# Kernel tuning notes

Hardware: AMD Instinct MI355X
Metric: run time of the kernel (lower is better)

Reference implementation:

```python
import jax, jax.numpy as jnp
import numpy as np

# Group structure (matches init_kwargs)
SIZES = np.array([16]*16 + [32]*32 + [64]*16)          # teacher_embedding_sizes_list
CHOICES = np.array([4]*16 + [8]*32 + [16]*16)          # max_choice_per_embedding
IN_DIM = int(SIZES.sum())                               # 2304
OUT_DIM = int(CHOICES.sum())                            # 576
W_TOTAL = int((SIZES * CHOICES).sum())                  # 25600
BATCH = 16384


def setup_inputs() -> dict:
    key = jax.random.key(0)
    k1, k2 = jax.random.split(key)
    x = jax.random.normal(k1, (BATCH, IN_DIM), dtype=jnp.float32)
    # TruncatedNormal(stddev=0.15) approximated with scaled normal
    weight = jax.random.normal(k2, (W_TOTAL, 1), dtype=jnp.float32) * 0.15
    bias = jnp.zeros((OUT_DIM,), dtype=jnp.float32)
    return {"x": x, "weight": weight, "bias": bias}


def reference(x, weight, bias):
    # Block-diagonal grouped GEMM: per-group slice of x times per-group weight
    # block reshaped to [size_i, choice_i], concatenated along features + bias.
    w_flat = weight[:, 0]
    outs = []
    w_idx = 0
    t_idx = 0
    for size, choice in zip(SIZES.tolist(), CHOICES.tolist()):
        x_slice = x[:, t_idx:t_idx + size]                       # [B, size]
        w_block = w_flat[w_idx:w_idx + size * choice].reshape(size, choice)
        outs.append(x_slice @ w_block)                           # [B, choice]
        w_idx += size * choice
        t_idx += size
    return jnp.concatenate(outs, axis=1) + bias
```

## Files before the change

### kernel.cpp

```cpp
#include <hip/hip_runtime.h>


#define BATCH   16384
#define IN_DIM  2304
#define OUT_DIM 576
#define CHUNKS  36
#define XS_LDW  68

__global__ __launch_bounds__(256) void fused_block_mm(
    const float* __restrict__ x, const float* __restrict__ w,
    const float* __restrict__ bias, float* __restrict__ out)
{
    __shared__ float xs[64 * XS_LDW];
    __shared__ float wd[64 * 16];

    const int tid = threadIdx.x;
    const int bx  = blockIdx.x;
    const int cj  = bx % CHUNKS;
    const int rt  = bx / CHUNKS;
    const int row_base = rt * 64;

    if (cj < 4) {
        const int wbase = cj * 256;
        #pragma unroll
        for (int i = 0; i < 4; ++i) {
            const int e = tid + i * 256, k = e >> 4, c = e & 15, b = k >> 4;
            wd[e] = ((c >> 2) == b)
                  ? w[wbase + b * 64 + ((k & 15) << 2) + (c & 3)] : 0.0f;
        }
    } else if (cj < 20) {
        const int wbase = 1024 + (cj - 4) * 512;
        #pragma unroll
        for (int i = 0; i < 4; ++i) {
            const int e = tid + i * 256, k = e >> 4, c = e & 15, b = k >> 5;
            wd[e] = ((c >> 3) == b)
                  ? w[wbase + b * 256 + ((k & 31) << 3) + (c & 7)] : 0.0f;
        }
    } else {
        const int wbase = 9216 + (cj - 20) * 1024;
        #pragma unroll
        for (int i = 0; i < 4; ++i) {
            const int e = tid + i * 256;
            wd[e] = w[wbase + e];
        }
    }

    const float* __restrict__ xsrc = x + (size_t)row_base * IN_DIM + cj * 64;
    #pragma unroll
    for (int i = 0; i < 4; ++i) {
        const int f = tid + i * 256, r = f >> 4, c = (f & 15) << 2;
        const float4 v = *reinterpret_cast<const float4*>(
            xsrc + (size_t)r * IN_DIM + c);
        *reinterpret_cast<float4*>(&xs[r * XS_LDW + c]) = v;
    }
    __syncthreads();

    const int wv   = __builtin_amdgcn_readfirstlane(tid >> 6);
    const int lane = tid & 63;
    const int ocol = cj * 16 + (wv << 2);

    float4 acc = make_float4(bias[ocol], bias[ocol + 1],
                             bias[ocol + 2], bias[ocol + 3]);

    const int xb = lane * XS_LDW;
    const int wb = wv << 2;
    #pragma unroll
    for (int k4 = 0; k4 < 16; ++k4) {
        const float4 xv = *reinterpret_cast<const float4*>(&xs[xb + (k4 << 2)]);
        const float4 w0 = *reinterpret_cast<const float4*>(&wd[(k4*4+0)*16 + wb]);
        const float4 w1 = *reinterpret_cast<const float4*>(&wd[(k4*4+1)*16 + wb]);
        const float4 w2 = *reinterpret_cast<const float4*>(&wd[(k4*4+2)*16 + wb]);
        const float4 w3 = *reinterpret_cast<const float4*>(&wd[(k4*4+3)*16 + wb]);
        acc.x += xv.x*w0.x + xv.y*w1.x + xv.z*w2.x + xv.w*w3.x;
        acc.y += xv.x*w0.y + xv.y*w1.y + xv.z*w2.y + xv.w*w3.y;
        acc.z += xv.x*w0.z + xv.y*w1.z + xv.z*w2.z + xv.w*w3.z;
        acc.w += xv.x*w0.w + xv.y*w1.w + xv.z*w2.w + xv.w*w3.w;
    }

    float* __restrict__ op = out + (size_t)(row_base + lane) * OUT_DIM + ocol;
    *reinterpret_cast<float4*>(op) = acc;
}

extern "C" void kernel_launch(void* const* d_in, const int* in_sizes, int n_in,
                              void* d_out, int out_size, void* d_ws, size_t ws_size,
                              hipStream_t stream) {
    const float* x    = (const float*)d_in[0];
    const float* w    = (const float*)d_in[1];
    const float* bias = (const float*)d_in[2];
    float* out        = (float*)d_out;

    const int row_tiles = BATCH / 64;
    fused_block_mm<<<dim3(CHUNKS * row_tiles), 256, 0, stream>>>(
        x, w, bias, out);
}
```

Before: 229.3 us.

## Skip zero blocks in block-diagonal chunks and register-tile four rows per thread

Each workgroup now covers 128 rows with 128 threads. Each thread computes a 4-row by 4-column tile, so every weight vector loaded from LDS is reused across four rows. For chunks that hold several small groups, a thread iterates only over the K range of its own diagonal block (16 or 32 instead of 64), which skips the zero-padded multiplies. The cost is more registers per thread, fewer threads per block, and a larger LDS tile.

```diff
diff --git a/kernel.cpp b/kernel.cpp
--- a/kernel.cpp
+++ b/kernel.cpp
@@ -6,79 +6,118 @@
 #define OUT_DIM 576
 #define CHUNKS  36
 #define XS_LDW  68
+#define ROWS_WG 128
 
-__global__ __launch_bounds__(256) void fused_block_mm(
+#define FMA_ROW(A, X)                                       \
+    A.x += X.x*w0.x + X.y*w1.x + X.z*w2.x + X.w*w3.x;       \
+    A.y += X.x*w0.y + X.y*w1.y + X.z*w2.y + X.w*w3.y;       \
+    A.z += X.x*w0.z + X.y*w1.z + X.z*w2.z + X.w*w3.z;       \
+    A.w += X.x*w0.w + X.y*w1.w + X.z*w2.w + X.w*w3.w;
+
+template<int NT>
+__device__ __forceinline__ void tile_fma(
+    const float* xq0, const float* xq1, const float* xq2, const float* xq3,
+    const float* wq, float4& a0, float4& a1, float4& a2, float4& a3)
+{
+#pragma unroll
+    for (int t = 0; t < NT; ++t) {
+        const int k = t << 2;
+        const float4 x0 = *reinterpret_cast<const float4*>(xq0 + k);
+        const float4 x1 = *reinterpret_cast<const float4*>(xq1 + k);
+        const float4 x2 = *reinterpret_cast<const float4*>(xq2 + k);
+        const float4 x3 = *reinterpret_cast<const float4*>(xq3 + k);
+        const float4 w0 = *reinterpret_cast<const float4*>(wq + (k + 0) * 16);
+        const float4 w1 = *reinterpret_cast<const float4*>(wq + (k + 1) * 16);
+        const float4 w2 = *reinterpret_cast<const float4*>(wq + (k + 2) * 16);
+        const float4 w3 = *reinterpret_cast<const float4*>(wq + (k + 3) * 16);
+        FMA_ROW(a0, x0)
+        FMA_ROW(a1, x1)
+        FMA_ROW(a2, x2)
+        FMA_ROW(a3, x3)
+    }
+}
+
+__global__ __launch_bounds__(128) void fused_block_mm(
     const float* __restrict__ x, const float* __restrict__ w,
     const float* __restrict__ bias, float* __restrict__ out)
 {
-    __shared__ float xs[64 * XS_LDW];
+    __shared__ float xs[ROWS_WG * XS_LDW];
     __shared__ float wd[64 * 16];
 
     const int tid = threadIdx.x;
     const int bx  = blockIdx.x;
     const int cj  = bx % CHUNKS;
     const int rt  = bx / CHUNKS;
-    const int row_base = rt * 64;
+    const int row_base = rt * ROWS_WG;
 
     if (cj < 4) {
         const int wbase = cj * 256;
         #pragma unroll
-        for (int i = 0; i < 4; ++i) {
-            const int e = tid + i * 256, k = e >> 4, c = e & 15, b = k >> 4;
+        for (int i = 0; i < 8; ++i) {
+            const int e = tid + i * 128, k = e >> 4, c = e & 15, b = k >> 4;
             wd[e] = ((c >> 2) == b)
                   ? w[wbase + b * 64 + ((k & 15) << 2) + (c & 3)] : 0.0f;
         }
     } else if (cj < 20) {
         const int wbase = 1024 + (cj - 4) * 512;
         #pragma unroll
-        for (int i = 0; i < 4; ++i) {
-            const int e = tid + i * 256, k = e >> 4, c = e & 15, b = k >> 5;
+        for (int i = 0; i < 8; ++i) {
+            const int e = tid + i * 128, k = e >> 4, c = e & 15, b = k >> 5;
             wd[e] = ((c >> 3) == b)
                   ? w[wbase + b * 256 + ((k & 31) << 3) + (c & 7)] : 0.0f;
         }
     } else {
         const int wbase = 9216 + (cj - 20) * 1024;
         #pragma unroll
-        for (int i = 0; i < 4; ++i) {
-            const int e = tid + i * 256;
+        for (int i = 0; i < 8; ++i) {
+            const int e = tid + i * 128;
             wd[e] = w[wbase + e];
         }
     }
 
     const float* __restrict__ xsrc = x + (size_t)row_base * IN_DIM + cj * 64;
     #pragma unroll
-    for (int i = 0; i < 4; ++i) {
-        const int f = tid + i * 256, r = f >> 4, c = (f & 15) << 2;
+    for (int i = 0; i < 16; ++i) {
+        const int f = tid + i * 128, r = f >> 4, c = (f & 15) << 2;
         const float4 v = *reinterpret_cast<const float4*>(
             xsrc + (size_t)r * IN_DIM + c);
         *reinterpret_cast<float4*>(&xs[r * XS_LDW + c]) = v;
     }
     __syncthreads();
 
-    const int wv   = __builtin_amdgcn_readfirstlane(tid >> 6);
+    const int wv   = tid >> 6;
     const int lane = tid & 63;
-    const int ocol = cj * 16 + (wv << 2);
+    const int rq   = lane & 15;
+    const int cq   = lane >> 4;
+    const int wb   = cq << 2;
+    const int row0 = wv * 64 + rq;
 
-    float4 acc = make_float4(bias[ocol], bias[ocol + 1],
-                             bias[ocol + 2], bias[ocol + 3]);
+    const float* xp0 = &xs[(row0 +  0) * XS_LDW];
+    const float* xp1 = &xs[(row0 + 16) * XS_LDW];
+    const float* xp2 = &xs[(row0 + 32) * XS_LDW];
+    const float* xp3 = &xs[(row0 + 48) * XS_LDW];
 
-    const int xb = lane * XS_LDW;
-    const int wb = wv << 2;
-    #pragma unroll
-    for (int k4 = 0; k4 < 16; ++k4) {
-        const float4 xv = *reinterpret_cast<const float4*>(&xs[xb + (k4 << 2)]);
-        const float4 w0 = *reinterpret_cast<const float4*>(&wd[(k4*4+0)*16 + wb]);
-        const float4 w1 = *reinterpret_cast<const float4*>(&wd[(k4*4+1)*16 + wb]);
-        const float4 w2 = *reinterpret_cast<const float4*>(&wd[(k4*4+2)*16 + wb]);
-        const float4 w3 = *reinterpret_cast<const float4*>(&wd[(k4*4+3)*16 + wb]);
-        acc.x += xv.x*w0.x + xv.y*w1.x + xv.z*w2.x + xv.w*w3.x;
-        acc.y += xv.x*w0.y + xv.y*w1.y + xv.z*w2.y + xv.w*w3.y;
-        acc.z += xv.x*w0.z + xv.y*w1.z + xv.z*w2.z + xv.w*w3.z;
-        acc.w += xv.x*w0.w + xv.y*w1.w + xv.z*w2.w + xv.w*w3.w;
+    const float4 bv = *reinterpret_cast<const float4*>(bias + cj * 16 + wb);
+    float4 a0 = bv, a1 = bv, a2 = bv, a3 = bv;
+
+    if (cj < 4) {
+        const int kb = cq << 4;
+        tile_fma<4>(xp0 + kb, xp1 + kb, xp2 + kb, xp3 + kb,
+                    &wd[wb + (kb << 4)], a0, a1, a2, a3);
+    } else if (cj < 20) {
+        const int kb = (cq >> 1) << 5;
+        tile_fma<8>(xp0 + kb, xp1 + kb, xp2 + kb, xp3 + kb,
+                    &wd[wb + (kb << 4)], a0, a1, a2, a3);
+    } else {
+        tile_fma<16>(xp0, xp1, xp2, xp3, &wd[wb], a0, a1, a2, a3);
     }
 
-    float* __restrict__ op = out + (size_t)(row_base + lane) * OUT_DIM + ocol;
-    *reinterpret_cast<float4*>(op) = acc;
+    float* __restrict__ op =
+        out + (size_t)(row_base + row0) * OUT_DIM + cj * 16 + wb;
+    *reinterpret_cast<float4*>(op)                = a0;
+    *reinterpret_cast<float4*>(op + 16 * OUT_DIM) = a1;
+    *reinterpret_cast<float4*>(op + 32 * OUT_DIM) = a2;
+    *reinterpret_cast<float4*>(op + 48 * OUT_DIM) = a3;
 }
 
 extern "C" void kernel_launch(void* const* d_in, const int* in_sizes, int n_in,
@@ -89,7 +128,7 @@
     const float* bias = (const float*)d_in[2];
     float* out        = (float*)d_out;
 
-    const int row_tiles = BATCH / 64;
-    fused_block_mm<<<dim3(CHUNKS * row_tiles), 256, 0, stream>>>(
+    const int row_tiles = BATCH / ROWS_WG;
+    fused_block_mm<<<dim3(CHUNKS * row_tiles), 128, 0, stream>>>(
         x, w, bias, out);
 }
```

After: 232.1 us. No clear change (+1.2%).
